# Kernel optimization log

Hardware: AMD Instinct MI355X
Metric: run time of the kernel (lower is better)

## Reference

```python
import jax, jax.numpy as jnp
import numpy as np

N = 50000   # function nodes
E = 100000  # edges per relation
H = 8       # heads
D = 96      # per-head dim (768 // 8)
L = 2       # conv layers
B = 256     # graphs in batch
C = 31      # num_classes + 1


def setup_inputs() -> dict:
    key = jax.random.key(0)
    ks = jax.random.split(key, 24)
    s = 0.05  # weight init scale to keep attention logits sane
    inp = {
        "function_feats": jax.random.normal(ks[0], (N, 768), jnp.float32),
        "w_src_calls": jax.random.normal(ks[1], (L, 768, 768), jnp.float32) * s,
        "b_src_calls": jnp.zeros((L, 768), jnp.float32),
        "w_dst_calls": jax.random.normal(ks[2], (L, 768, 768), jnp.float32) * s,
        "b_dst_calls": jnp.zeros((L, 768), jnp.float32),
        "attn_calls": jax.random.normal(ks[3], (L, H, D), jnp.float32) * s,
        "w_src_cb": jax.random.normal(ks[4], (L, 768, 768), jnp.float32) * s,
        "b_src_cb": jnp.zeros((L, 768), jnp.float32),
        "w_dst_cb": jax.random.normal(ks[5], (L, 768, 768), jnp.float32) * s,
        "b_dst_cb": jnp.zeros((L, 768), jnp.float32),
        "attn_cb": jax.random.normal(ks[6], (L, H, D), jnp.float32) * s,
        "fc1_w": jax.random.normal(ks[7], (768, 256), jnp.float32) * s,
        "fc1_b": jnp.zeros((256,), jnp.float32),
        "fc2_w": jax.random.normal(ks[8], (256, C), jnp.float32) * s,
        "fc2_b": jnp.zeros((C,), jnp.float32),
        "calls_src": jax.random.randint(ks[9], (E,), 0, N),
        "calls_dst": jax.random.randint(ks[10], (E,), 0, N),
        "cb_src": jax.random.randint(ks[11], (E,), 0, N),
        "cb_dst": jax.random.randint(ks[12], (E,), 0, N),
        "graph_start_idx": jnp.sort(jax.random.randint(ks[13], (B,), 0, N)),
        "labels": jax.random.randint(ks[14], (B,), 0, C),
    }
    return inp


def _gatv2(h, Ws, bs, Wd, bd, attn, src, dst):
    # DGL GATv2Conv: e_ij = attn . leaky_relu(W_src h_i + W_dst h_j); softmax over in-edges of j
    fs = (h @ Ws + bs).reshape(N, H, D)
    fd = (h @ Wd + bd).reshape(N, H, D)
    e = jax.nn.leaky_relu(fs[src] + fd[dst], negative_slope=0.2)  # [E,H,D]
    score = jnp.einsum('ehd,hd->eh', e, attn)                      # [E,H]
    mx = jax.ops.segment_max(score, dst, num_segments=N)           # [N,H]
    ex = jnp.exp(score - mx[dst])
    den = jax.ops.segment_sum(ex, dst, num_segments=N)
    alpha = ex / den[dst]                                          # edge softmax
    return jax.ops.segment_sum(fs[src] * alpha[..., None], dst, num_segments=N)  # [N,H,D]


def reference(function_feats, w_src_calls, b_src_calls, w_dst_calls, b_dst_calls,
              attn_calls, w_src_cb, b_src_cb, w_dst_cb, b_dst_cb, attn_cb,
              fc1_w, fc1_b, fc2_w, fc2_b,
              calls_src, calls_dst, cb_src, cb_dst, graph_start_idx, labels):
    h = function_feats
    for l in range(L):
        o = _gatv2(h, w_src_calls[l], b_src_calls[l], w_dst_calls[l], b_dst_calls[l],
                   attn_calls[l], calls_src, calls_dst)
        o = o + _gatv2(h, w_src_cb[l], b_src_cb[l], w_dst_cb[l], b_dst_cb[l],
                       attn_cb[l], cb_src, cb_dst)  # HeteroGraphConv 'sum' aggregate
        h = o.reshape(N, H * D) + h                  # residual
    func_embed = h[graph_start_idx]                  # [B,768] gather first node per graph
    logits = jax.nn.relu(func_embed @ fc1_w + fc1_b) @ fc2_w + fc2_b  # [B,C]
    logp = jax.nn.log_softmax(logits, axis=-1)
    loss = -jnp.mean(jnp.take_along_axis(logp, labels[:, None], axis=1))
    return (loss, logits)
```

## Files before the change

kernel.cpp:

```cpp
#include <hip/hip_runtime.h>
#include <hip/hip_bf16.h>
#include <math.h>

#define N_NODES 50000
#define NE      100000
#define FDIM    768
#define NFUSE   3072
#define NB      256
#define NC      31

#define A1_CAP  16384
#define N1_CAP  4096
#define NBLK    ((N_NODES + 255) / 256)
#define EB      ((NE + 255) / 256)
#define GTN     12

#define TWT_BLOCKS  (8 * 576)
#define BIAS_BLOCKS 24
#define CVT_BLOCKS  512
#define SETUP_BLOCKS (TWT_BLOCKS + BIAS_BLOCKS + CVT_BLOCKS)
#define SETUPH_BLOCKS (SETUP_BLOCKS + 2 * EB)

typedef __hip_bfloat16 bf16;
typedef __attribute__((ext_vector_type(8))) short bf16x8;
typedef __attribute__((ext_vector_type(4))) float f32x4;

__device__ inline float u2f(unsigned short u) { return __uint_as_float(((unsigned int)u) << 16); }
__device__ inline unsigned short f2u(float f) { return __bfloat16_as_ushort(__float2bfloat16(f)); }

__device__ inline void load_lds16(const void* g, void* l) {
    __builtin_amdgcn_global_load_lds(
        (const __attribute__((address_space(1))) void*)g,
        (__attribute__((address_space(3))) void*)l, 16, 0, 0);
}

__global__ __launch_bounds__(256) void markA_kernel(const int* __restrict__ gsi,
                                                    const int* __restrict__ src0,
                                                    const int* __restrict__ dst0,
                                                    const int* __restrict__ src1,
                                                    const int* __restrict__ dst1,
                                                    int* __restrict__ fL1,
                                                    int* __restrict__ fA1,
                                                    int* __restrict__ list0,
                                                    int* __restrict__ cnts) {
    const int t = threadIdx.x, b = blockIdx.x;
    if (b == 0) {
        const int n = gsi[t];
        fL1[n] = 1; fA1[n] = 1;
        const bool first = (t == 0) || (gsi[t - 1] != n);
        if (first) {
            const int p = atomicAdd(&cnts[2], 1);
            if (p < 256) list0[p] = n;
        }
        return;
    }
    __shared__ int g[256];
    g[t] = gsi[t];
    __syncthreads();
    const int eb = b - 1;
    const int r = (eb >= EB) ? 1 : 0;
    const int e = (eb - r * EB) * 256 + t;
    if (e >= NE) return;
    const int d = (r ? dst1 : dst0)[e];
    int lo = 0, hi = 256;
    while (lo < hi) { const int mid = (lo + hi) >> 1; if (g[mid] < d) lo = mid + 1; else hi = mid; }
    if (lo < 256 && g[lo] == d) {
        const int s = (r ? src1 : src0)[e];
        fL1[s] = 1; fA1[s] = 1;
    }
}

__global__ __launch_bounds__(256) void markB_kernel(const int* __restrict__ src0,
                                                    const int* __restrict__ dst0,
                                                    const int* __restrict__ src1,
                                                    const int* __restrict__ dst1,
                                                    const int* __restrict__ fL1,
                                                    int* __restrict__ fA1) {
    const int e = blockIdx.x * 256 + threadIdx.x;
    if (e >= NE) return;
    const int r = blockIdx.y;
    if (fL1[(r ? dst1 : dst0)[e]]) fA1[(r ? src1 : src0)[e]] = 1;
}

__global__ __launch_bounds__(256) void compact_kernel(const int* __restrict__ fA1,
                                                      const int* __restrict__ fL1,
                                                      int* __restrict__ list1, int* __restrict__ idx1,
                                                      int* __restrict__ list2, int* __restrict__ idx2,
                                                      int* __restrict__ cnts) {
    const int n = blockIdx.x * 256 + threadIdx.x;
    if (n >= N_NODES) return;
    if (fA1[n]) {
        const int p = atomicAdd(&cnts[0], 1);
        if (p < A1_CAP) { list1[p] = n; idx1[n] = p; } else idx1[n] = 0;
    }
    if (fL1[n]) {
        const int p = atomicAdd(&cnts[1], 1);
        if (p < N1_CAP) { list2[p] = n; idx2[n] = p; } else idx2[n] = 0;
    }
}

__global__ __launch_bounds__(256) void setup_kernel(const float* __restrict__ w_sc,
                                                    const float* __restrict__ w_dc,
                                                    const float* __restrict__ w_scb,
                                                    const float* __restrict__ w_dcb,
                                                    const float* __restrict__ b_sc,
                                                    const float* __restrict__ b_dc,
                                                    const float* __restrict__ b_scb,
                                                    const float* __restrict__ b_dcb,
                                                    const float* __restrict__ feats,
                                                    const int* __restrict__ list,
                                                    const int* __restrict__ pcnt,
                                                    bf16* __restrict__ WtFl,
                                                    float* __restrict__ pb,
                                                    bf16* __restrict__ h,
                                                    const int* __restrict__ dst0,
                                                    const int* __restrict__ dst1,
                                                    const int* __restrict__ fL1,
                                                    const int* __restrict__ idx2,
                                                    int* __restrict__ dega) {
    __shared__ float tile[32][33];
    const int b = blockIdx.x;
    const int t = threadIdx.x;
    if (b < TWT_BLOCKS) {
        const int z = b / 576, cell = b % 576;
        const int l = z >> 2, sel2 = z & 3;
        const float* src;
        if (sel2 == 0) src = w_sc; else if (sel2 == 1) src = w_scb;
        else if (sel2 == 2) src = w_dc; else src = w_dcb;
        src += (size_t)l * FDIM * FDIM;
        bf16* dst = WtFl + (size_t)z * FDIM * FDIM;
        const int tx = t & 31, ty = t >> 5;
        const int x0 = (cell % 24) * 32, y0 = (cell / 24) * 32;
#pragma unroll
        for (int q = 0; q < 4; ++q)
            tile[ty + q * 8][tx] = src[(size_t)(y0 + ty + q * 8) * FDIM + x0 + tx];
        __syncthreads();
#pragma unroll
        for (int q = 0; q < 4; ++q)
            dst[(size_t)(x0 + ty + q * 8) * FDIM + y0 + tx] = __float2bfloat16(tile[tx][ty + q * 8]);
    } else if (b < TWT_BLOCKS + BIAS_BLOCKS) {
        const int idx = (b - TWT_BLOCKS) * 256 + t;
        const int l = idx / NFUSE, c = idx % NFUSE;
        const int sel2 = c / FDIM, off = c % FDIM;
        const float* src;
        if (sel2 == 0) src = b_sc; else if (sel2 == 1) src = b_scb;
        else if (sel2 == 2) src = b_dc; else src = b_dcb;
        pb[idx] = src[l * FDIM + off];
    } else if (b < SETUP_BLOCKS) {
        int c = *pcnt; if (c > A1_CAP) c = A1_CAP;
        for (int i = b - TWT_BLOCKS - BIAS_BLOCKS; i < c; i += CVT_BLOCKS) {
            const int n = list[i];
            const float* s = feats + (size_t)n * FDIM;
            bf16* d = h + (size_t)n * FDIM;
            for (int k = t; k < FDIM; k += 256) d[k] = __float2bfloat16(s[k]);
        }
    } else {
        const int eb = b - SETUP_BLOCKS;
        const int r = (eb >= EB) ? 1 : 0;
        const int e = (eb - r * EB) * 256 + t;
        if (e < NE) {
            const int d = (r ? dst1 : dst0)[e];
            if (fL1[d]) atomicAdd(&dega[r * N1_CAP + idx2[d]], 1);
        }
    }
}

__global__ __launch_bounds__(256) void scana_kernel(const int* __restrict__ dega,
                                                    int* __restrict__ rowpa,
                                                    int* __restrict__ cursora) {
    __shared__ int part[256];
    const int t = threadIdx.x;
    for (int r = 0; r < 2; ++r) {
        const int base = r * N1_CAP;
        int loc[16];
        int s = 0;
#pragma unroll
        for (int q = 0; q < 16; ++q) { loc[q] = dega[base + t * 16 + q]; s += loc[q]; }
        part[t] = s;
        __syncthreads();
        for (int o = 1; o < 256; o <<= 1) {
            int x = (t >= o) ? part[t - o] : 0;
            __syncthreads();
            part[t] += x;
            __syncthreads();
        }
        int run = part[t] - s;
        const int rbase = r * (N1_CAP + 1);
#pragma unroll
        for (int q = 0; q < 16; ++q) {
            rowpa[rbase + t * 16 + q] = run;
            cursora[base + t * 16 + q] = run;
            run += loc[q];
        }
        if (t == 255) rowpa[rbase + N1_CAP] = run;
        __syncthreads();
    }
}

__global__ __launch_bounds__(256) void scattera_kernel(const int* __restrict__ dst0,
                                                       const int* __restrict__ dst1,
                                                       const int* __restrict__ fL1,
                                                       const int* __restrict__ idx2,
                                                       int* __restrict__ cursora,
                                                       int* __restrict__ eida) {
    const int e = blockIdx.x * 256 + threadIdx.x;
    if (e >= NE) return;
    const int r = blockIdx.y;
    const int d = (r ? dst1 : dst0)[e];
    if (fL1[d]) {
        const int p = atomicAdd(&cursora[r * N1_CAP + idx2[d]], 1);
        eida[(size_t)r * NE + p] = e;
    }
}

__global__ __launch_bounds__(256) void gemm2(const bf16* __restrict__ A,
                                             const bf16* __restrict__ Wt,
                                             const float* __restrict__ pb,
                                             bf16* __restrict__ C,
                                             const int* __restrict__ rlA,
                                             const int* __restrict__ cntAp, int capA,
                                             const int* __restrict__ rlB,
                                             const int* __restrict__ cntBp, int capB,
                                             const int* __restrict__ idxmap,
                                             int blocksA) {
    int bid = blockIdx.x;
    const int* rowlist;
    int cnt, col0;
    if (bid < blocksA) {
        rowlist = rlA; cnt = *cntAp; if (cnt > capA) cnt = capA; col0 = 0;
    } else {
        bid -= blocksA;
        rowlist = rlB; cnt = *cntBp; if (cnt > capB) cnt = capB; col0 = 1536;
    }
    const int tm = bid / GTN, tn = bid % GTN;
    const int m0 = tm * 128, n0 = tn * 128;
    if (m0 >= cnt) return;

    __shared__ __align__(16) short Abuf[128 * 64];
    __shared__ __align__(16) short Bbuf[128 * 64];
    const int t = threadIdx.x;
    const int wid = t >> 6, lane = t & 63;
    const int wr = wid >> 1, wc = wid & 1;
    const int lr = lane & 15, lk = lane >> 4;

    const f32x4 zero4 = {0.f, 0.f, 0.f, 0.f};
    f32x4 acc[4][4];
#pragma unroll
    for (int i = 0; i < 4; ++i)
#pragma unroll
        for (int j = 0; j < 4; ++j) acc[i][j] = zero4;

    int arow[4], brow[4], acol[4], ldsoff[4];
#pragma unroll
    for (int i = 0; i < 4; ++i) {
        const int s = i * 256 + t;
        const int rr = s >> 3, pch = s & 7;
        int ri = m0 + rr; if (ri >= cnt) ri = cnt - 1;
        arow[i] = rowlist[ri];
        brow[i] = col0 + n0 + rr;
        acol[i] = (pch ^ (rr & 7)) << 3;
        ldsoff[i] = (i * 256 + wid * 64) * 16;
    }

    for (int kt = 0; kt < FDIM / 64; ++kt) {
        const int k0 = kt * 64;
#pragma unroll
        for (int i = 0; i < 4; ++i) {
            load_lds16(A + (size_t)arow[i] * FDIM + k0 + acol[i], (char*)Abuf + ldsoff[i]);
            load_lds16(Wt + (size_t)brow[i] * FDIM + k0 + acol[i], (char*)Bbuf + ldsoff[i]);
        }
        __syncthreads();
#pragma unroll
        for (int kh = 0; kh < 2; ++kh) {
            bf16x8 av[4], bv[4];
            const int c = kh * 4 + lk;
#pragma unroll
            for (int i = 0; i < 4; ++i) {
                const int mm = wr * 64 + i * 16 + lr;
                av[i] = *(const bf16x8*)((const char*)Abuf + mm * 128 + ((c ^ (mm & 7)) << 4));
            }
#pragma unroll
            for (int j = 0; j < 4; ++j) {
                const int nn = wc * 64 + j * 16 + lr;
                bv[j] = *(const bf16x8*)((const char*)Bbuf + nn * 128 + ((c ^ (nn & 7)) << 4));
            }
#pragma unroll
            for (int i = 0; i < 4; ++i)
#pragma unroll
                for (int j = 0; j < 4; ++j)
                    acc[i][j] = __builtin_amdgcn_mfma_f32_16x16x32_bf16(bv[j], av[i], acc[i][j], 0, 0, 0);
        }
        __syncthreads();
    }

#pragma unroll
    for (int i = 0; i < 4; ++i) {
        const int row = m0 + wr * 64 + i * 16 + lr;
        if (row < cnt) {
            const int crow = idxmap[rowlist[row]];
#pragma unroll
            for (int j = 0; j < 4; ++j) {
                const int col = col0 + n0 + wc * 64 + j * 16 + lk * 4;
                const float4 b4 = *(const float4*)(pb + col);
                ushort4 w;
                w.x = f2u(acc[i][j][0] + b4.x);
                w.y = f2u(acc[i][j][1] + b4.y);
                w.z = f2u(acc[i][j][2] + b4.z);
                w.w = f2u(acc[i][j][3] + b4.w);
                *(ushort4*)(C + (size_t)crow * NFUSE + col) = w;
            }
        }
    }
}

__device__ inline void att_accum(const bf16* __restrict__ fsd, const int* __restrict__ idxsrc,
                                 int fdrow, int lane, const float* __restrict__ attn,
                                 int beg, int end,
                                 const int* __restrict__ eid, const int* __restrict__ src,
                                 int fs_off, int fd_off, float* __restrict__ out) {
    float fdv[12], atv[12];
    {
        const ushort4* pfd = (const ushort4*)(fsd + (size_t)fdrow * NFUSE + fd_off + lane * 12);
        const ushort4 d0 = pfd[0], d1 = pfd[1], d2 = pfd[2];
        fdv[0] = u2f(d0.x); fdv[1] = u2f(d0.y); fdv[2] = u2f(d0.z); fdv[3] = u2f(d0.w);
        fdv[4] = u2f(d1.x); fdv[5] = u2f(d1.y); fdv[6] = u2f(d1.z); fdv[7] = u2f(d1.w);
        fdv[8] = u2f(d2.x); fdv[9] = u2f(d2.y); fdv[10] = u2f(d2.z); fdv[11] = u2f(d2.w);
        const float4* pat = (const float4*)(attn + lane * 12);
        const float4 a0 = pat[0], a1 = pat[1], a2 = pat[2];
        atv[0] = a0.x; atv[1] = a0.y; atv[2] = a0.z; atv[3] = a0.w;
        atv[4] = a1.x; atv[5] = a1.y; atv[6] = a1.z; atv[7] = a1.w;
        atv[8] = a2.x; atv[9] = a2.y; atv[10] = a2.z; atv[11] = a2.w;
    }
    float m = -INFINITY, den = 0.f;
    float acc[12];
#pragma unroll
    for (int j = 0; j < 12; ++j) acc[j] = 0.f;

    for (int i = beg; i < end; ++i) {
        const int e = eid[i];
        const ushort4* pf = (const ushort4*)(fsd + (size_t)idxsrc[src[e]] * NFUSE + fs_off + lane * 12);
        const ushort4 a0 = pf[0], a1 = pf[1], a2 = pf[2];
        float fsv[12];
        fsv[0] = u2f(a0.x); fsv[1] = u2f(a0.y); fsv[2] = u2f(a0.z); fsv[3] = u2f(a0.w);
        fsv[4] = u2f(a1.x); fsv[5] = u2f(a1.y); fsv[6] = u2f(a1.z); fsv[7] = u2f(a1.w);
        fsv[8] = u2f(a2.x); fsv[9] = u2f(a2.y); fsv[10] = u2f(a2.z); fsv[11] = u2f(a2.w);
        float p = 0.f;
#pragma unroll
        for (int j = 0; j < 12; ++j) {
            float x = fsv[j] + fdv[j];
            x = (x > 0.f) ? x : 0.2f * x;
            p += x * atv[j];
        }
        p += __shfl_xor(p, 1);
        p += __shfl_xor(p, 2);
        p += __shfl_xor(p, 4);
        if (p > m) {
            const float sc = expf(m - p);
            den *= sc;
#pragma unroll
            for (int j = 0; j < 12; ++j) acc[j] *= sc;
            m = p;
        }
        const float w = expf(p - m);
        den += w;
#pragma unroll
        for (int j = 0; j < 12; ++j) acc[j] += w * fsv[j];
    }
    const float inv = (den > 0.f) ? 1.f / den : 0.f;
#pragma unroll
    for (int j = 0; j < 12; ++j) out[j] = acc[j] * inv;
}

__global__ __launch_bounds__(256) void aggL_kernel(const bf16* __restrict__ fsd,
                                                   const int* __restrict__ idx1,
                                                   const float* __restrict__ attn0,
                                                   const float* __restrict__ attn1,
                                                   const int* __restrict__ rowpa,
                                                   const int* __restrict__ eida,
                                                   const int* __restrict__ src0,
                                                   const int* __restrict__ src1,
                                                   bf16* __restrict__ h,
                                                   const int* __restrict__ list2,
                                                   const int* __restrict__ pcnt) {
    const int wid = threadIdx.x >> 6;
    const int lane = threadIdx.x & 63;
    int cnt = *pcnt; if (cnt > N1_CAP) cnt = N1_CAP;
    const int i = blockIdx.x * 4 + wid;
    if (i >= cnt) return;
    const int n = list2[i];
    const int fdrow = idx1[n];

    float a0[12], a1[12];
    att_accum(fsd, idx1, fdrow, lane, attn0, rowpa[i], rowpa[i + 1],
              eida, src0, 0, 1536, a0);
    att_accum(fsd, idx1, fdrow, lane, attn1, rowpa[(N1_CAP + 1) + i], rowpa[(N1_CAP + 1) + i + 1],
              eida + NE, src1, 768, 2304, a1);

    const size_t base = (size_t)n * FDIM + lane * 12;
    const ushort4* ph = (const ushort4*)(h + base);
    const ushort4 h0 = ph[0], h1 = ph[1], h2 = ph[2];
    ushort4 r0, r1, r2;
    r0.x = f2u(u2f(h0.x) + a0[0] + a1[0]);  r0.y = f2u(u2f(h0.y) + a0[1] + a1[1]);
    r0.z = f2u(u2f(h0.z) + a0[2] + a1[2]);  r0.w = f2u(u2f(h0.w) + a0[3] + a1[3]);
    r1.x = f2u(u2f(h1.x) + a0[4] + a1[4]);  r1.y = f2u(u2f(h1.y) + a0[5] + a1[5]);
    r1.z = f2u(u2f(h1.z) + a0[6] + a1[6]);  r1.w = f2u(u2f(h1.w) + a0[7] + a1[7]);
    r2.x = f2u(u2f(h2.x) + a0[8] + a1[8]);  r2.y = f2u(u2f(h2.y) + a0[9] + a1[9]);
    r2.z = f2u(u2f(h2.z) + a0[10] + a1[10]); r2.w = f2u(u2f(h2.w) + a0[11] + a1[11]);
    ((ushort4*)(h + base))[0] = r0; ((ushort4*)(h + base))[1] = r1; ((ushort4*)(h + base))[2] = r2;
}

__global__ __launch_bounds__(256) void agghead_kernel(const bf16* __restrict__ fsd,
                                                      const int* __restrict__ idx2,
                                                      const float* __restrict__ attn0,
                                                      const float* __restrict__ attn1,
                                                      const int* __restrict__ rowpa,
                                                      const int* __restrict__ eida,
                                                      const int* __restrict__ src0,
                                                      const int* __restrict__ src1,
                                                      const bf16* __restrict__ h,
                                                      const int* __restrict__ gsi,
                                                      const float* __restrict__ fc1w,
                                                      const float* __restrict__ fc1b,
                                                      const float* __restrict__ fc2w,
                                                      const float* __restrict__ fc2b,
                                                      float* __restrict__ out) {
    __shared__ float a0s[FDIM], a1s[FDIM], fe[FDIM];
    __shared__ float hid[256];
    const int b = blockIdx.x, t = threadIdx.x;
    const int n = gsi[b];
    const int wv = t >> 6, lane = t & 63;
    if (wv < 2) {
        const int j = idx2[n];
        const int rb = wv * (N1_CAP + 1);
        float a[12];
        att_accum(fsd, idx2, j, lane, wv ? attn1 : attn0,
                  rowpa[rb + j], rowpa[rb + j + 1],
                  eida + (size_t)wv * NE, wv ? src1 : src0,
                  wv ? 768 : 0, wv ? 2304 : 1536, a);
        float* dl = wv ? a1s : a0s;
#pragma unroll
        for (int q = 0; q < 12; ++q) dl[lane * 12 + q] = a[q];
    }
    __syncthreads();
    for (int d = t; d < FDIM; d += 256)
        fe[d] = u2f(__bfloat16_as_ushort(h[(size_t)n * FDIM + d])) + a0s[d] + a1s[d];
    __syncthreads();
    float acc = fc1b[t];
    for (int k = 0; k < FDIM; ++k) acc += fe[k] * fc1w[k * 256 + t];
    hid[t] = (acc > 0.f) ? acc : 0.f;
    __syncthreads();
    if (t < NC) {
        float a2 = fc2b[t];
        for (int k = 0; k < 256; ++k) a2 += hid[k] * fc2w[k * NC + t];
        out[1 + b * NC + t] = a2;
    }
}

__global__ __launch_bounds__(256) void loss_kernel(const float* __restrict__ logits,
                                                   const int* __restrict__ labels,
                                                   float* __restrict__ out) {
    __shared__ float red[256];
    const int b = threadIdx.x;
    float m = -INFINITY;
    for (int c = 0; c < NC; ++c) m = fmaxf(m, logits[b * NC + c]);
    float sum = 0.f;
    for (int c = 0; c < NC; ++c) sum += expf(logits[b * NC + c] - m);
    const float lse = m + logf(sum);
    const float ll = logits[b * NC + labels[b]];
    red[b] = lse - ll;
    __syncthreads();
    for (int s = 128; s > 0; s >>= 1) {
        if (b < s) red[b] += red[b + s];
        __syncthreads();
    }
    if (b == 0) out[0] = red[0] / (float)NB;
}

extern "C" void kernel_launch(void* const* d_in, const int* in_sizes, int n_in,
                              void* d_out, int out_size, void* d_ws, size_t ws_size,
                              hipStream_t stream) {
    const float* feats = (const float*)d_in[0];
    const float* fc1w  = (const float*)d_in[11];
    const float* fc1b  = (const float*)d_in[12];
    const float* fc2w  = (const float*)d_in[13];
    const float* fc2b  = (const float*)d_in[14];
    const int* src0    = (const int*)d_in[15];
    const int* dst0    = (const int*)d_in[16];
    const int* src1    = (const int*)d_in[17];
    const int* dst1    = (const int*)d_in[18];
    const int* gsi     = (const int*)d_in[19];
    const int* labels  = (const int*)d_in[20];

    const size_t NF = (size_t)N_NODES * FDIM;
    const size_t WSZ = (size_t)FDIM * FDIM;
    char* p = (char*)d_ws;
    bf16* h    = (bf16*)p;  p += NF * 2;
    bf16* fsd  = (bf16*)p;  p += (size_t)A1_CAP * NFUSE * 2;
    bf16* WtFl = (bf16*)p;  p += 8 * WSZ * 2;
    float* pb  = (float*)p; p += 2 * NFUSE * 4;
    int* fA1  = (int*)p;    p += (size_t)N_NODES * 4;
    int* fL1  = (int*)p;    p += (size_t)N_NODES * 4;
    int* cnts = (int*)p;    p += 64 * 4;
    int* dega = (int*)p;    p += 2 * (size_t)N1_CAP * 4;
    const size_t zero_bytes = (2 * (size_t)N_NODES + 64 + 2 * (size_t)N1_CAP) * 4;
    int* idx1  = (int*)p;   p += (size_t)N_NODES * 4;
    int* idx2  = (int*)p;   p += (size_t)N_NODES * 4;
    int* list1 = (int*)p;   p += (size_t)A1_CAP * 4;
    int* list2 = (int*)p;   p += (size_t)N1_CAP * 4;
    int* list0 = (int*)p;   p += 256 * 4;
    int* rowpa = (int*)p;   p += 2 * ((size_t)N1_CAP + 1) * 4;
    int* cursora = (int*)p; p += 2 * (size_t)N1_CAP * 4;
    int* eida  = (int*)p;   p += 2 * (size_t)NE * 4;

    hipMemsetAsync(fA1, 0, zero_bytes, stream);
    markA_kernel<<<1 + 2 * EB, 256, 0, stream>>>(gsi, src0, dst0, src1, dst1, fL1, fA1, list0, cnts);
    markB_kernel<<<dim3(EB, 2), 256, 0, stream>>>(src0, dst0, src1, dst1, fL1, fA1);
    compact_kernel<<<NBLK, 256, 0, stream>>>(fA1, fL1, list1, idx1, list2, idx2, cnts);
    setup_kernel<<<SETUPH_BLOCKS, 256, 0, stream>>>(
        (const float*)d_in[1], (const float*)d_in[3], (const float*)d_in[6], (const float*)d_in[8],
        (const float*)d_in[2], (const float*)d_in[4], (const float*)d_in[7], (const float*)d_in[9],
        feats, list1, &cnts[0], WtFl, pb, h, dst0, dst1, fL1, idx2, dega);
    scana_kernel<<<1, 256, 0, stream>>>(dega, rowpa, cursora);
    scattera_kernel<<<dim3(EB, 2), 256, 0, stream>>>(dst0, dst1, fL1, idx2, cursora, eida);

    const int blocksA0 = (A1_CAP / 128) * GTN;
    const int blocksB0 = (N1_CAP / 128) * GTN;
    const int blocksA1 = (N1_CAP / 128) * GTN;
    const int blocksB1 = (256 / 128) * GTN;

    gemm2<<<blocksA0 + blocksB0, 256, 0, stream>>>(
        h, WtFl, pb, fsd,
        list1, &cnts[0], A1_CAP, list2, &cnts[1], N1_CAP, idx1, blocksA0);
    aggL_kernel<<<(N1_CAP + 3) / 4, 256, 0, stream>>>(
        fsd, idx1, (const float*)d_in[5], (const float*)d_in[10],
        rowpa, eida, src0, src1, h, list2, &cnts[1]);

    gemm2<<<blocksA1 + blocksB1, 256, 0, stream>>>(
        h, WtFl + 4 * WSZ, pb + NFUSE, fsd,
        list2, &cnts[1], N1_CAP, list0, &cnts[2], 256, idx2, blocksA1);
    agghead_kernel<<<NB, 256, 0, stream>>>(
        fsd, idx2, (const float*)d_in[5] + FDIM, (const float*)d_in[10] + FDIM,
        rowpa, eida, src0, src1, h, gsi, fc1w, fc1b, fc2w, fc2b, (float*)d_out);

    loss_kernel<<<1, 256, 0, stream>>>((float*)d_out + 1, labels, (float*)d_out);
}
```

Measured before the change: 159.5 us.

## Fold compaction, scan, scatter and loss into neighbouring kernels to cut launches

Node compaction now happens inside the mark kernels through atomicExch first-set detection, which removes the separate compact pass over all nodes. The prefix scan runs in the last-finishing setup block, found with an atomic counter. The edge scatter runs as extra blocks prepended to the first GEMM launch, and the loss is computed by the last agghead block. This drops four kernel launches and their serialization gaps, at the cost of atomic contention, last-block patterns that rely on device-scope atomic visibility, and GEMM blocks sharing the grid with the scatter blocks.

After: 254.4 us. 1.6x slower.

```diff
diff --git a/kernel.cpp b/kernel.cpp
--- a/kernel.cpp
+++ b/kernel.cpp
@@ -11,15 +11,15 @@
 
 #define A1_CAP  16384
 #define N1_CAP  4096
-#define NBLK    ((N_NODES + 255) / 256)
 #define EB      ((NE + 255) / 256)
+#define SCT     (2 * EB)
 #define GTN     12
 
 #define TWT_BLOCKS  (8 * 576)
 #define BIAS_BLOCKS 24
 #define CVT_BLOCKS  512
 #define SETUP_BLOCKS (TWT_BLOCKS + BIAS_BLOCKS + CVT_BLOCKS)
-#define SETUPH_BLOCKS (SETUP_BLOCKS + 2 * EB)
+#define SETUPH_BLOCKS (SETUP_BLOCKS + SCT)
 
 typedef __hip_bfloat16 bf16;
 typedef __attribute__((ext_vector_type(8))) short bf16x8;
@@ -27,6 +27,16 @@
 
 __device__ inline float u2f(unsigned short u) { return __uint_as_float(((unsigned int)u) << 16); }
 __device__ inline unsigned short f2u(float f) { return __bfloat16_as_ushort(__float2bfloat16(f)); }
+
+__device__ inline int aload_i(const int* p) {
+    return __hip_atomic_load(p, __ATOMIC_RELAXED, __HIP_MEMORY_SCOPE_AGENT);
+}
+__device__ inline float aload_f(const float* p) {
+    return __hip_atomic_load(p, __ATOMIC_RELAXED, __HIP_MEMORY_SCOPE_AGENT);
+}
+__device__ inline void astore_f(float* p, float v) {
+    __hip_atomic_store(p, v, __ATOMIC_RELAXED, __HIP_MEMORY_SCOPE_AGENT);
+}
 
 __device__ inline void load_lds16(const void* g, void* l) {
     __builtin_amdgcn_global_load_lds(
@@ -41,12 +51,21 @@
                                                     const int* __restrict__ dst1,
                                                     int* __restrict__ fL1,
                                                     int* __restrict__ fA1,
+                                                    int* __restrict__ list1, int* __restrict__ idx1,
+                                                    int* __restrict__ list2, int* __restrict__ idx2,
                                                     int* __restrict__ list0,
                                                     int* __restrict__ cnts) {
     const int t = threadIdx.x, b = blockIdx.x;
     if (b == 0) {
         const int n = gsi[t];
-        fL1[n] = 1; fA1[n] = 1;
+        if (atomicExch(&fL1[n], 1) == 0) {
+            const int p = atomicAdd(&cnts[1], 1);
+            if (p < N1_CAP) { list2[p] = n; idx2[n] = p; } else idx2[n] = 0;
+        }
+        if (atomicExch(&fA1[n], 1) == 0) {
+            const int p = atomicAdd(&cnts[0], 1);
+            if (p < A1_CAP) { list1[p] = n; idx1[n] = p; } else idx1[n] = 0;
+        }
         const bool first = (t == 0) || (gsi[t - 1] != n);
         if (first) {
             const int p = atomicAdd(&cnts[2], 1);
@@ -66,7 +85,14 @@
     while (lo < hi) { const int mid = (lo + hi) >> 1; if (g[mid] < d) lo = mid + 1; else hi = mid; }
     if (lo < 256 && g[lo] == d) {
         const int s = (r ? src1 : src0)[e];
-        fL1[s] = 1; fA1[s] = 1;
+        if (atomicExch(&fL1[s], 1) == 0) {
+            const int p = atomicAdd(&cnts[1], 1);
+            if (p < N1_CAP) { list2[p] = s; idx2[s] = p; } else idx2[s] = 0;
+        }
+        if (atomicExch(&fA1[s], 1) == 0) {
+            const int p = atomicAdd(&cnts[0], 1);
+            if (p < A1_CAP) { list1[p] = s; idx1[s] = p; } else idx1[s] = 0;
+        }
     }
 }
 
@@ -75,27 +101,18 @@
                                                     const int* __restrict__ src1,
                                                     const int* __restrict__ dst1,
                                                     const int* __restrict__ fL1,
-                                                    int* __restrict__ fA1) {
+                                                    int* __restrict__ fA1,
+                                                    int* __restrict__ list1, int* __restrict__ idx1,
+                                                    int* __restrict__ cnts) {
     const int e = blockIdx.x * 256 + threadIdx.x;
     if (e >= NE) return;
     const int r = blockIdx.y;
-    if (fL1[(r ? dst1 : dst0)[e]]) fA1[(r ? src1 : src0)[e]] = 1;
-}
-
-__global__ __launch_bounds__(256) void compact_kernel(const int* __restrict__ fA1,
-                                                      const int* __restrict__ fL1,
-                                                      int* __restrict__ list1, int* __restrict__ idx1,
-                                                      int* __restrict__ list2, int* __restrict__ idx2,
-                                                      int* __restrict__ cnts) {
-    const int n = blockIdx.x * 256 + threadIdx.x;
-    if (n >= N_NODES) return;
-    if (fA1[n]) {
-        const int p = atomicAdd(&cnts[0], 1);
-        if (p < A1_CAP) { list1[p] = n; idx1[n] = p; } else idx1[n] = 0;
-    }
-    if (fL1[n]) {
-        const int p = atomicAdd(&cnts[1], 1);
-        if (p < N1_CAP) { list2[p] = n; idx2[n] = p; } else idx2[n] = 0;
+    if (fL1[(r ? dst1 : dst0)[e]]) {
+        const int s = (r ? src1 : src0)[e];
+        if (atomicExch(&fA1[s], 1) == 0) {
+            const int p = atomicAdd(&cnts[0], 1);
+            if (p < A1_CAP) { list1[p] = s; idx1[s] = p; } else idx1[s] = 0;
+        }
     }
 }
 
@@ -117,7 +134,10 @@
                                                     const int* __restrict__ dst1,
                                                     const int* __restrict__ fL1,
                                                     const int* __restrict__ idx2,
-                                                    int* __restrict__ dega) {
+                                                    int* __restrict__ dega,
+                                                    int* __restrict__ cnts,
+                                                    int* __restrict__ rowpa,
+                                                    int* __restrict__ cursora) {
     __shared__ float tile[32][33];
     const int b = blockIdx.x;
     const int t = threadIdx.x;
@@ -163,53 +183,38 @@
             if (fL1[d]) atomicAdd(&dega[r * N1_CAP + idx2[d]], 1);
         }
     }
-}
-
-__global__ __launch_bounds__(256) void scana_kernel(const int* __restrict__ dega,
-                                                    int* __restrict__ rowpa,
-                                                    int* __restrict__ cursora) {
-    __shared__ int part[256];
-    const int t = threadIdx.x;
-    for (int r = 0; r < 2; ++r) {
-        const int base = r * N1_CAP;
-        int loc[16];
-        int s = 0;
-#pragma unroll
-        for (int q = 0; q < 16; ++q) { loc[q] = dega[base + t * 16 + q]; s += loc[q]; }
-        part[t] = s;
-        __syncthreads();
-        for (int o = 1; o < 256; o <<= 1) {
-            int x = (t >= o) ? part[t - o] : 0;
+
+    __syncthreads();
+    __shared__ int amlast;
+    if (t == 0) amlast = (atomicAdd(&cnts[8], 1) == SETUPH_BLOCKS - 1) ? 1 : 0;
+    __syncthreads();
+    if (amlast) {
+        __shared__ int part[256];
+        for (int r = 0; r < 2; ++r) {
+            const int base = r * N1_CAP;
+            int loc[16];
+            int s = 0;
+#pragma unroll
+            for (int q = 0; q < 16; ++q) { loc[q] = aload_i(&dega[base + t * 16 + q]); s += loc[q]; }
+            part[t] = s;
             __syncthreads();
-            part[t] += x;
+            for (int o = 1; o < 256; o <<= 1) {
+                int x = (t >= o) ? part[t - o] : 0;
+                __syncthreads();
+                part[t] += x;
+                __syncthreads();
+            }
+            int run = part[t] - s;
+            const int rbase = r * (N1_CAP + 1);
+#pragma unroll
+            for (int q = 0; q < 16; ++q) {
+                rowpa[rbase + t * 16 + q] = run;
+                cursora[base + t * 16 + q] = run;
+                run += loc[q];
+            }
+            if (t == 255) rowpa[rbase + N1_CAP] = run;
             __syncthreads();
         }
-        int run = part[t] - s;
-        const int rbase = r * (N1_CAP + 1);
-#pragma unroll
-        for (int q = 0; q < 16; ++q) {
-            rowpa[rbase + t * 16 + q] = run;
-            cursora[base + t * 16 + q] = run;
-            run += loc[q];
-        }
-        if (t == 255) rowpa[rbase + N1_CAP] = run;
-        __syncthreads();
-    }
-}
-
-__global__ __launch_bounds__(256) void scattera_kernel(const int* __restrict__ dst0,
-                                                       const int* __restrict__ dst1,
-                                                       const int* __restrict__ fL1,
-                                                       const int* __restrict__ idx2,
-                                                       int* __restrict__ cursora,
-                                                       int* __restrict__ eida) {
-    const int e = blockIdx.x * 256 + threadIdx.x;
-    if (e >= NE) return;
-    const int r = blockIdx.y;
-    const int d = (r ? dst1 : dst0)[e];
-    if (fL1[d]) {
-        const int p = atomicAdd(&cursora[r * N1_CAP + idx2[d]], 1);
-        eida[(size_t)r * NE + p] = e;
     }
 }
 
@@ -222,8 +227,28 @@
                                              const int* __restrict__ rlB,
                                              const int* __restrict__ cntBp, int capB,
                                              const int* __restrict__ idxmap,
-                                             int blocksA) {
+                                             int blocksA,
+                                             int sct,
+                                             const int* __restrict__ dst0,
+                                             const int* __restrict__ dst1,
+                                             const int* __restrict__ fL1,
+                                             const int* __restrict__ idx2,
+                                             int* __restrict__ cursora,
+                                             int* __restrict__ eida) {
     int bid = blockIdx.x;
+    if (bid < sct) {
+        const int r = (bid >= EB) ? 1 : 0;
+        const int e = (bid - r * EB) * 256 + threadIdx.x;
+        if (e < NE) {
+            const int d = (r ? dst1 : dst0)[e];
+            if (fL1[d]) {
+                const int p = atomicAdd(&cursora[r * N1_CAP + idx2[d]], 1);
+                eida[(size_t)r * NE + p] = e;
+            }
+        }
+        return;
+    }
+    bid -= sct;
     const int* rowlist;
     int cnt, col0;
     if (bid < blocksA) {
@@ -423,6 +448,8 @@
                                                       const float* __restrict__ fc1b,
                                                       const float* __restrict__ fc2w,
                                                       const float* __restrict__ fc2b,
+                                                      const int* __restrict__ labels,
+                                                      int* __restrict__ cnts,
                                                       float* __restrict__ out) {
     __shared__ float a0s[FDIM], a1s[FDIM], fe[FDIM];
     __shared__ float hid[256];
@@ -432,14 +459,14 @@
     if (wv < 2) {
         const int j = idx2[n];
         const int rb = wv * (N1_CAP + 1);
-        float a[12];
+        float v[12];
         att_accum(fsd, idx2, j, lane, wv ? attn1 : attn0,
                   rowpa[rb + j], rowpa[rb + j + 1],
                   eida + (size_t)wv * NE, wv ? src1 : src0,
-                  wv ? 768 : 0, wv ? 2304 : 1536, a);
+                  wv ? 768 : 0, wv ? 2304 : 1536, v);
         float* dl = wv ? a1s : a0s;
 #pragma unroll
-        for (int q = 0; q < 12; ++q) dl[lane * 12 + q] = a[q];
+        for (int q = 0; q < 12; ++q) dl[lane * 12 + q] = v[q];
     }
     __syncthreads();
     for (int d = t; d < FDIM; d += 256)
@@ -452,38 +479,41 @@
     if (t < NC) {
         float a2 = fc2b[t];
         for (int k = 0; k < 256; ++k) a2 += hid[k] * fc2w[k * NC + t];
-        out[1 + b * NC + t] = a2;
-    }
-}
-
-__global__ __launch_bounds__(256) void loss_kernel(const float* __restrict__ logits,
-                                                   const int* __restrict__ labels,
-                                                   float* __restrict__ out) {
-    __shared__ float red[256];
-    const int b = threadIdx.x;
-    float m = -INFINITY;
-    for (int c = 0; c < NC; ++c) m = fmaxf(m, logits[b * NC + c]);
-    float sum = 0.f;
-    for (int c = 0; c < NC; ++c) sum += expf(logits[b * NC + c] - m);
-    const float lse = m + logf(sum);
-    const float ll = logits[b * NC + labels[b]];
-    red[b] = lse - ll;
-    __syncthreads();
-    for (int s = 128; s > 0; s >>= 1) {
-        if (b < s) red[b] += red[b + s];
+        astore_f(&out[1 + b * NC + t], a2);
+    }
+
+    __syncthreads();
+    __shared__ int amlast;
+    if (t == 0) amlast = (atomicAdd(&cnts[9], 1) == NB - 1) ? 1 : 0;
+    __syncthreads();
+    if (amlast) {
+        __shared__ float red[256];
+        float m = -INFINITY;
+        float lg[NC];
+#pragma unroll
+        for (int c = 0; c < NC; ++c) {
+            lg[c] = aload_f(&out[1 + t * NC + c]);
+            m = fmaxf(m, lg[c]);
+        }
+        float sum = 0.f;
+#pragma unroll
+        for (int c = 0; c < NC; ++c) sum += expf(lg[c] - m);
+        const float lse = m + logf(sum);
+        const float ll = lg[labels[t]];
+        red[t] = lse - ll;
         __syncthreads();
-    }
-    if (b == 0) out[0] = red[0] / (float)NB;
+        for (int s = 128; s > 0; s >>= 1) {
+            if (t < s) red[t] += red[t + s];
+            __syncthreads();
+        }
+        if (t == 0) out[0] = red[0] / (float)NB;
+    }
 }
 
 extern "C" void kernel_launch(void* const* d_in, const int* in_sizes, int n_in,
                               void* d_out, int out_size, void* d_ws, size_t ws_size,
                               hipStream_t stream) {
     const float* feats = (const float*)d_in[0];
-    const float* fc1w  = (const float*)d_in[11];
-    const float* fc1b  = (const float*)d_in[12];
-    const float* fc2w  = (const float*)d_in[13];
-    const float* fc2b  = (const float*)d_in[14];
     const int* src0    = (const int*)d_in[15];
     const int* dst0    = (const int*)d_in[16];
     const int* src1    = (const int*)d_in[17];
@@ -513,34 +543,35 @@
     int* eida  = (int*)p;   p += 2 * (size_t)NE * 4;
 
     hipMemsetAsync(fA1, 0, zero_bytes, stream);
-    markA_kernel<<<1 + 2 * EB, 256, 0, stream>>>(gsi, src0, dst0, src1, dst1, fL1, fA1, list0, cnts);
-    markB_kernel<<<dim3(EB, 2), 256, 0, stream>>>(src0, dst0, src1, dst1, fL1, fA1);
-    compact_kernel<<<NBLK, 256, 0, stream>>>(fA1, fL1, list1, idx1, list2, idx2, cnts);
+    markA_kernel<<<1 + SCT, 256, 0, stream>>>(gsi, src0, dst0, src1, dst1,
+                                              fL1, fA1, list1, idx1, list2, idx2, list0, cnts);
+    markB_kernel<<<dim3(EB, 2), 256, 0, stream>>>(src0, dst0, src1, dst1, fL1, fA1,
+                                                  list1, idx1, cnts);
     setup_kernel<<<SETUPH_BLOCKS, 256, 0, stream>>>(
         (const float*)d_in[1], (const float*)d_in[3], (const float*)d_in[6], (const float*)d_in[8],
         (const float*)d_in[2], (const float*)d_in[4], (const float*)d_in[7], (const float*)d_in[9],
-        feats, list1, &cnts[0], WtFl, pb, h, dst0, dst1, fL1, idx2, dega);
-    scana_kernel<<<1, 256, 0, stream>>>(dega, rowpa, cursora);
-    scattera_kernel<<<dim3(EB, 2), 256, 0, stream>>>(dst0, dst1, fL1, idx2, cursora, eida);
+        feats, list1, &cnts[0], WtFl, pb, h, dst0, dst1, fL1, idx2, dega, cnts, rowpa, cursora);
 
     const int blocksA0 = (A1_CAP / 128) * GTN;
     const int blocksB0 = (N1_CAP / 128) * GTN;
     const int blocksA1 = (N1_CAP / 128) * GTN;
     const int blocksB1 = (256 / 128) * GTN;
 
-    gemm2<<<blocksA0 + blocksB0, 256, 0, stream>>>(
+    gemm2<<<SCT + blocksA0 + blocksB0, 256, 0, stream>>>(
         h, WtFl, pb, fsd,
-        list1, &cnts[0], A1_CAP, list2, &cnts[1], N1_CAP, idx1, blocksA0);
+        list1, &cnts[0], A1_CAP, list2, &cnts[1], N1_CAP, idx1, blocksA0,
+        SCT, dst0, dst1, fL1, idx2, cursora, eida);
     aggL_kernel<<<(N1_CAP + 3) / 4, 256, 0, stream>>>(
         fsd, idx1, (const float*)d_in[5], (const float*)d_in[10],
         rowpa, eida, src0, src1, h, list2, &cnts[1]);
-
     gemm2<<<blocksA1 + blocksB1, 256, 0, stream>>>(
         h, WtFl + 4 * WSZ, pb + NFUSE, fsd,
-        list2, &cnts[1], N1_CAP, list0, &cnts[2], 256, idx2, blocksA1);
+        list2, &cnts[1], N1_CAP, list0, &cnts[2], 256, idx2, blocksA1,
+        0, dst0, dst1, fL1, idx2, cursora, eida);
     agghead_kernel<<<NB, 256, 0, stream>>>(
         fsd, idx2, (const float*)d_in[5] + FDIM, (const float*)d_in[10] + FDIM,
-        rowpa, eida, src0, src1, h, gsi, fc1w, fc1b, fc2w, fc2b, (float*)d_out);
-
-    loss_kernel<<<1, 256, 0, stream>>>((float*)d_out + 1, labels, (float*)d_out);
-}
+        rowpa, eida, src0, src1, h, gsi,
+        (const float*)d_in[11], (const float*)d_in[12],
+        (const float*)d_in[13], (const float*)d_in[14],
+        labels, cnts, (float*)d_out);
+}
```
